# Performance work log

Measured on AMD Instinct MI355X. Metric: run time of the kernel, lower is better.

Reference implementation:

```python
import jax, jax.numpy as jnp
import numpy as np

N_NODES = 1_000_000
N_EDGES = 5_000_000
N_GRAPHS = 4096
HIDDEN = 16


def transform(x):
    # Transform wrapper: fn=tanh, then nan_to_num(nan=0, posinf=10, neginf=-10).clamp(-10, 10)
    y = jnp.tanh(x)
    y = jnp.nan_to_num(y, nan=0.0, posinf=10.0, neginf=-10.0)
    return jnp.clip(y, -10.0, 10.0)


def setup_inputs() -> dict:
    key = jax.random.key(0)
    ks = jax.random.split(key, 10)
    x = jax.random.normal(ks[0], (N_NODES, 3), dtype=jnp.float32)
    edge_index = jax.random.randint(ks[1], (2, N_EDGES), 0, N_NODES, dtype=jnp.int32)
    batch = jnp.sort(jax.random.randint(ks[2], (N_NODES,), 0, N_GRAPHS, dtype=jnp.int32))
    s1 = 1.0 / np.sqrt(3.0)
    s2 = 1.0 / np.sqrt(HIDDEN)
    s3 = 1.0 / np.sqrt(2 * HIDDEN)
    w1 = jax.random.uniform(ks[3], (3, HIDDEN), jnp.float32, -s1, s1)
    b1 = jax.random.uniform(ks[4], (HIDDEN,), jnp.float32, -s1, s1)
    w2 = jax.random.uniform(ks[5], (HIDDEN, HIDDEN), jnp.float32, -s2, s2)
    b2 = jax.random.uniform(ks[6], (HIDDEN,), jnp.float32, -s2, s2)
    w3 = jax.random.uniform(ks[7], (2 * HIDDEN, 1), jnp.float32, -s3, s3)
    b3 = jax.random.uniform(ks[8], (1,), jnp.float32, -s3, s3)
    return {"x": x, "edge_index": edge_index, "batch": batch,
            "w1": w1, "b1": b1, "w2": w2, "b2": b2, "w3": w3, "b3": b3}


def reference(x, edge_index, batch, w1, b1, w2, b2, w3, b3):
    n_nodes = x.shape[0]
    h = transform(x @ w1 + b1)                                  # [N, H]
    row, col = edge_index[0], edge_index[1]
    # degree of each destination node (row), clamped to >= 1
    deg = jax.ops.segment_sum(jnp.ones((row.shape[0],), x.dtype), row,
                              num_segments=n_nodes)             # [N]
    deg = jnp.maximum(deg, 1.0)
    # gather source features, scatter-add to destinations, normalize
    agg = jax.ops.segment_sum(h[col], row, num_segments=n_nodes)  # [N, H]
    agg = agg / deg[:, None]
    h = transform(agg @ w2 + b2)                                # [N, H]
    # per-graph mean and max pooling
    cnt = jax.ops.segment_sum(jnp.ones((n_nodes,), x.dtype), batch,
                              num_segments=N_GRAPHS)            # [G]
    h_sum = jax.ops.segment_sum(h, batch, num_segments=N_GRAPHS)  # [G, H]
    h_mean = h_sum / jnp.maximum(cnt, 1.0)[:, None]
    h_max = jax.ops.segment_max(h, batch, num_segments=N_GRAPHS)  # [G, H]
    h_max = jnp.where(jnp.isneginf(h_max), 0.0, h_max)
    pooled = jnp.concatenate([h_mean, h_max], axis=1)           # [G, 2H]
    out = jax.nn.sigmoid(pooled @ w3 + b3)                      # [G, 1]
    return out.squeeze(-1)
```

## Files before the change

kernel.cpp:

```cpp
#include <hip/hip_runtime.h>
#include <hip/hip_bf16.h>
#include <hip/hip_fp16.h>

static constexpr int NN = 1000000;
static constexpr int NE = 5000000;
static constexpr int NG = 4096;
static constexpr int BIN_SH = 8;
static constexpr int BIN_SZ = 1 << BIN_SH;
static constexpr int NB = (NN + BIN_SZ - 1) >> BIN_SH;
static constexpr int CAP_SH = 11;
static constexpr int CAP = 1 << CAP_SH;
static constexpr int EPB = 16384;
static constexpr int EPW = EPB / 1024;
static constexpr int BIN_BLOCKS = (NE + EPB - 1) / EPB;
static constexpr int CHUNK = 512;
static constexpr float KEXP = 2.8853900817779268f;

__device__ __forceinline__ float exp2_fast(float x) {
#if __has_builtin(__builtin_amdgcn_exp2f)
    return __builtin_amdgcn_exp2f(x);
#else
    return exp2f(x);
#endif
}

__device__ __forceinline__ float tanh_scaled(float s) {
    float e = exp2_fast(s);
    return fmaf(-2.0f, __frcp_rn(e + 1.0f), 1.0f);
}

__device__ __forceinline__ float fast_tanh(float x) {
    float e = __expf(2.0f * x);
    return 1.0f - 2.0f * __fdividef(1.0f, e + 1.0f);
}

__global__ __launch_bounds__(1024) void bin_scatter_k(
    const int* __restrict__ row, const int* __restrict__ col,
    const float* __restrict__ x,
    int* __restrict__ binCursor, unsigned int* __restrict__ pack,
    __half* __restrict__ xh)
{
    __shared__ int hist[NB];
    for (int i = blockIdx.x * 1024 + threadIdx.x; i < NN; i += BIN_BLOCKS * 1024) {
        union { __half2 h2[2]; uint2 u; } o;
        o.h2[0] = __floats2half2_rn(x[3 * i + 0], x[3 * i + 1]);
        o.h2[1] = __floats2half2_rn(x[3 * i + 2], 0.0f);
        *reinterpret_cast<uint2*>(xh + 4 * (size_t)i) = o.u;
    }

    for (int i = threadIdx.x; i < NB; i += 1024) hist[i] = 0;
    __syncthreads();
    int base = blockIdx.x * EPB;

    int r[EPW], c[EPW];
    bool val[EPW];
#pragma unroll
    for (int k = 0; k < EPW; ++k) {
        int e = base + k * 1024 + threadIdx.x;
        val[k] = e < NE;
        r[k] = val[k] ? row[e] : 0;
        c[k] = val[k] ? col[e] : 0;
    }
#pragma unroll
    for (int k = 0; k < EPW; ++k)
        if (val[k]) atomicAdd(&hist[r[k] >> BIN_SH], 1);
    __syncthreads();
    for (int i = threadIdx.x; i < NB; i += 1024) {
        int cc = hist[i];
        hist[i] = cc ? ((i << CAP_SH) + atomicAdd(&binCursor[i], cc)) : 0;
    }
    __syncthreads();
    int pos[EPW];
#pragma unroll
    for (int k = 0; k < EPW; ++k)
        if (val[k]) pos[k] = atomicAdd(&hist[r[k] >> BIN_SH], 1);
#pragma unroll
    for (int k = 0; k < EPW; ++k)
        if (val[k]) pack[pos[k]] = ((unsigned int)(r[k] & (BIN_SZ - 1)) << 20)
                                   | (unsigned int)c[k];
}

#define PREFETCH_CHUNK(CS2, GX0, GX1, RL0, RL1)                                   \
    {                                                                             \
        RL0 = RL1 = -1;                                                           \
        int cs2_ = (CS2);                                                         \
        if (cs2_ < ee) {                                                          \
            int mm_ = min(CHUNK, ee - cs2_);                                      \
            int o0_ = tid, o1_ = 256 + tid;                                       \
            if (o0_ < mm_) {                                                      \
                unsigned int p_ = pack[cs2_ + o0_];                               \
                RL0 = (int)(p_ >> 20);                                            \
                GX0 = *reinterpret_cast<const uint2*>(xh + 4 * (size_t)(p_ & 0xFFFFFu)); \
            }                                                                     \
            if (o1_ < mm_) {                                                      \
                unsigned int p_ = pack[cs2_ + o1_];                               \
                RL1 = (int)(p_ >> 20);                                            \
                GX1 = *reinterpret_cast<const uint2*>(xh + 4 * (size_t)(p_ & 0xFFFFFu)); \
            }                                                                     \
        }                                                                         \
    }

__global__ __launch_bounds__(256) void bucket_agg_k(
    const unsigned int* __restrict__ pack,
    const int* __restrict__ binCursor,
    const __half* __restrict__ xh,
    const int* __restrict__ batch,
    const float* __restrict__ w1,
    const float* __restrict__ b1,
    const float* __restrict__ w2,
    const float* __restrict__ b2,
    float* __restrict__ h_sum,
    unsigned int* __restrict__ h_max,
    int* __restrict__ cnt)
{
    __shared__ uint4 pay[CHUNK * 2];
    __shared__ int scnt[BIN_SZ];
    __shared__ int sstart[BIN_SZ];
    __shared__ int wsum[4];

    int tid = threadIdx.x;
    int lane = tid & 63, wid = tid >> 6;
    int b = blockIdx.x;
    int nodeBase = b << BIN_SH;
    int nNodes = min(BIN_SZ, NN - nodeBase);
    int es = b << CAP_SH;
    int ee = es + binCursor[b];

    float b1s[16];
#pragma unroll
    for (int j = 0; j < 16; ++j) b1s[j] = b1[j] * KEXP;

    __half2 acc8[8];
#pragma unroll
    for (int q = 0; q < 8; ++q) acc8[q] = __half2half2(__float2half(0.0f));
    int dg = 0;

    uint2 gxA0, gxA1, gxB0, gxB1;
    int rlA0, rlA1, rlB0, rlB1;
    PREFETCH_CHUNK(es,          gxA0, gxA1, rlA0, rlA1);
    PREFETCH_CHUNK(es + CHUNK,  gxB0, gxB1, rlB0, rlB1);

    for (int cs = es; cs < ee; cs += CHUNK) {
        int m = min(CHUNK, ee - cs);
        scnt[tid] = 0;
        __syncthreads();

        if (rlA0 >= 0) atomicAdd(&scnt[rlA0], 1);
        if (rlA1 >= 0) atomicAdd(&scnt[rlA1], 1);

        uint2 gxC0, gxC1;
        int rlC0, rlC1;
        PREFETCH_CHUNK(cs + 2 * CHUNK, gxC0, gxC1, rlC0, rlC1);
        __syncthreads();

        int v = scnt[tid];
        int sc = v;
#pragma unroll
        for (int off = 1; off < 64; off <<= 1) {
            int u = __shfl_up(sc, off);
            if (lane >= off) sc += u;
        }
        if (lane == 63) wsum[wid] = sc;
        __syncthreads();
        int pre = 0;
#pragma unroll
        for (int w = 0; w < 4; ++w) pre += (w < wid) ? wsum[w] : 0;
        int ex = pre + sc - v;
        sstart[tid] = ex;
        scnt[tid] = ex;
        __syncthreads();

#pragma unroll
        for (int k = 0; k < 2; ++k) {
            int rlk = k ? rlA1 : rlA0;
            if (rlk >= 0) {
                union { uint2 u; __half2 h2[2]; } xi;
                xi.u = k ? gxA1 : gxA0;
                float2 x01 = __half22float2(xi.h2[0]);
                float xs0 = x01.x * KEXP;
                float xs1 = x01.y * KEXP;
                float xs2 = __low2float(xi.h2[1]) * KEXP;
                union { __half2 h2[8]; uint4 u[2]; } o;
#pragma unroll
                for (int q = 0; q < 8; ++q) {
                    float va = fmaf(xs2, w1[32 + 2 * q], fmaf(xs1, w1[16 + 2 * q],
                               fmaf(xs0, w1[2 * q], b1s[2 * q])));
                    float vb = fmaf(xs2, w1[33 + 2 * q], fmaf(xs1, w1[17 + 2 * q],
                               fmaf(xs0, w1[2 * q + 1], b1s[2 * q + 1])));
                    o.h2[q] = __floats2half2_rn(tanh_scaled(va), tanh_scaled(vb));
                }
                int pos = atomicAdd(&scnt[rlk], 1);
                pay[2 * pos + 0] = o.u[0];
                pay[2 * pos + 1] = o.u[1];
            }
        }
        __syncthreads();

        if (tid < nNodes) {
            int s0 = sstart[tid];
            int e0 = (tid < 255) ? sstart[tid + 1] : m;
            dg += e0 - s0;
            for (int e = s0; e < e0; ++e) {
                union { uint4 u; __half2 h2[4]; } ua, ub;
                ua.u = pay[2 * e + 0];
                ub.u = pay[2 * e + 1];
#pragma unroll
                for (int q = 0; q < 4; ++q) {
                    acc8[q] = __hadd2(acc8[q], ua.h2[q]);
                    acc8[4 + q] = __hadd2(acc8[4 + q], ub.h2[q]);
                }
            }
        }
        __syncthreads();

        gxA0 = gxB0; gxA1 = gxB1; rlA0 = rlB0; rlA1 = rlB1;
        gxB0 = gxC0; gxB1 = gxC1; rlB0 = rlC0; rlB1 = rlC1;
    }

    if (tid < nNodes) {
        float acc[16];
#pragma unroll
        for (int q = 0; q < 8; ++q) {
            float2 f = __half22float2(acc8[q]);
            acc[2 * q + 0] = f.x;
            acc[2 * q + 1] = f.y;
        }
        float inv = 1.0f / fmaxf((float)dg, 1.0f);
        float s[16];
#pragma unroll
        for (int j = 0; j < 16; ++j) s[j] = b2[j];
#pragma unroll
        for (int k = 0; k < 16; ++k) {
            float a = acc[k] * inv;
#pragma unroll
            for (int j = 0; j < 16; ++j) s[j] = fmaf(a, w2[16 * k + j], s[j]);
        }
        float m[16];
#pragma unroll
        for (int j = 0; j < 16; ++j) { s[j] = fast_tanh(s[j]); m[j] = s[j]; }

        int g = batch[nodeBase + tid];
        int gp = __shfl_up(g, 1);
        int head = (lane == 0) || (g != gp);
        unsigned long long hm = __ballot(head != 0);

        int f = head;
#pragma unroll
        for (int off = 1; off < 64; off <<= 1) {
            int fu = __shfl_up(f, off);
            bool take = (lane >= off) && (f == 0);
#pragma unroll
            for (int j = 0; j < 16; ++j) {
                float su = __shfl_up(s[j], off);
                float mu = __shfl_up(m[j], off);
                if (take) { s[j] += su; m[j] = fmaxf(m[j], mu); }
            }
            if (lane >= off) f |= fu;
        }

        int hnext = __shfl_down(head, 1);
        bool is_last = (lane == 63) || (hnext != 0);
        if (is_last) {
            unsigned long long below = hm & (~0ULL >> (63 - lane));
            int start = 63 - __clzll(below);
            int seglen = lane - start + 1;
#pragma unroll
            for (int j = 0; j < 16; ++j) {
                unsafeAtomicAdd(&h_sum[16 * g + j], s[j]);
                atomicMax(&h_max[16 * g + j], __float_as_uint(m[j] + 2.0f));
            }
            atomicAdd(&cnt[g], seglen);
        }
    }
}

__global__ __launch_bounds__(256) void out_k(
    const float* __restrict__ h_sum,
    const unsigned int* __restrict__ h_max,
    const int* __restrict__ cnt,
    const float* __restrict__ w3,
    const float* __restrict__ b3,
    float* __restrict__ out)
{
    int g = blockIdx.x * 256 + threadIdx.x;
    if (g >= NG) return;
    float invc = 1.0f / fmaxf((float)cnt[g], 1.0f);
    float acc = b3[0];
#pragma unroll
    for (int j = 0; j < 16; ++j) {
        float mean = h_sum[16 * g + j] * invc;
        unsigned int e = h_max[16 * g + j];
        float mx = (e == 0u) ? 0.0f : (__uint_as_float(e) - 2.0f);
        acc = fmaf(mean, w3[j], fmaf(mx, w3[16 + j], acc));
    }
    out[g] = 1.0f / (1.0f + __expf(-acc));
}

extern "C" void kernel_launch(void* const* d_in, const int* in_sizes, int n_in,
                              void* d_out, int out_size, void* d_ws, size_t ws_size,
                              hipStream_t stream)
{
    const float* x   = (const float*)d_in[0];
    const int*   ei  = (const int*)d_in[1];
    const int*   bat = (const int*)d_in[2];
    const float* w1  = (const float*)d_in[3];
    const float* b1  = (const float*)d_in[4];
    const float* w2  = (const float*)d_in[5];
    const float* b2  = (const float*)d_in[6];
    const float* w3  = (const float*)d_in[7];
    const float* b3  = (const float*)d_in[8];
    float* out = (float*)d_out;

    char* ws = (char*)d_ws;
    size_t off = 0;
    int* binCursor = (int*)(ws + off);         off += 16384;
    float* h_sum  = (float*)(ws + off);        off += (size_t)NG * 16 * 4;
    unsigned int* h_max = (unsigned int*)(ws + off); off += (size_t)NG * 16 * 4;
    int* cnt      = (int*)(ws + off);          off += (size_t)NG * 4;
    size_t zero_bytes = off;
    unsigned int* pack = (unsigned int*)(ws + off); off += (size_t)NB * CAP * 4;
    __half* xh    = (__half*)(ws + off);       off += (size_t)NN * 4 * 2;

    hipMemsetAsync(d_ws, 0, zero_bytes, stream);

    bin_scatter_k<<<BIN_BLOCKS, 1024, 0, stream>>>(ei, ei + NE, x, binCursor, pack, xh);
    bucket_agg_k<<<NB, 256, 0, stream>>>(pack, binCursor, xh, bat,
                                         w1, b1, w2, b2, h_sum, h_max, cnt);
    out_k<<<(NG + 255) / 256, 256, 0, stream>>>(h_sum, h_max, cnt, w3, b3, out);
}
```

Baseline: 187.5 us.

## Process each node bin with a single wavefront instead of a whole block

Each 256-node bin is now handled by one 64-lane wavefront, with four bins per block. Each wave has private LDS scratch, and every block-wide __syncthreads is replaced by a wave barrier. Each lane handles four nodes, chunks shrink to 128 edges, and the prefix scan over bin counts becomes a single-wave scan over int4 groups. This removes block-level synchronisation, at the cost of more serial work per lane, more registers for four accumulators, and load imbalance between waves within a block.

```diff
diff --git a/kernel.cpp b/kernel.cpp
--- a/kernel.cpp
+++ b/kernel.cpp
@@ -13,7 +13,7 @@
 static constexpr int EPB = 16384;
 static constexpr int EPW = EPB / 1024;
 static constexpr int BIN_BLOCKS = (NE + EPB - 1) / EPB;
-static constexpr int CHUNK = 512;
+static constexpr int CHUNKW = 128;
 static constexpr float KEXP = 2.8853900817779268f;
 
 __device__ __forceinline__ float exp2_fast(float x) {
@@ -80,20 +80,19 @@
                                    | (unsigned int)c[k];
 }
 
-#define PREFETCH_CHUNK(CS2, GX0, GX1, RL0, RL1)                                   \
+#define PREFETCH_W(CS2, GX0, GX1, RL0, RL1)                                       \
     {                                                                             \
         RL0 = RL1 = -1;                                                           \
         int cs2_ = (CS2);                                                         \
         if (cs2_ < ee) {                                                          \
-            int mm_ = min(CHUNK, ee - cs2_);                                      \
-            int o0_ = tid, o1_ = 256 + tid;                                       \
-            if (o0_ < mm_) {                                                      \
-                unsigned int p_ = pack[cs2_ + o0_];                               \
+            int mm_ = min(CHUNKW, ee - cs2_);                                     \
+            if (lane < mm_) {                                                     \
+                unsigned int p_ = pack[cs2_ + lane];                              \
                 RL0 = (int)(p_ >> 20);                                            \
                 GX0 = *reinterpret_cast<const uint2*>(xh + 4 * (size_t)(p_ & 0xFFFFFu)); \
             }                                                                     \
-            if (o1_ < mm_) {                                                      \
-                unsigned int p_ = pack[cs2_ + o1_];                               \
+            if (64 + lane < mm_) {                                                \
+                unsigned int p_ = pack[cs2_ + 64 + lane];                         \
                 RL1 = (int)(p_ >> 20);                                            \
                 GX1 = *reinterpret_cast<const uint2*>(xh + 4 * (size_t)(p_ & 0xFFFFFu)); \
             }                                                                     \
@@ -113,14 +112,18 @@
     unsigned int* __restrict__ h_max,
     int* __restrict__ cnt)
 {
-    __shared__ uint4 pay[CHUNK * 2];
-    __shared__ int scnt[BIN_SZ];
-    __shared__ int sstart[BIN_SZ];
-    __shared__ int wsum[4];
+    __shared__ uint4 payA[4][CHUNKW * 2];
+    __shared__ int scntA[4][BIN_SZ];
+    __shared__ int sstartA[4][BIN_SZ];
 
     int tid = threadIdx.x;
     int lane = tid & 63, wid = tid >> 6;
-    int b = blockIdx.x;
+    uint4* pay = payA[wid];
+    int* scnt = scntA[wid];
+    int* sstart = sstartA[wid];
+
+    int b = blockIdx.x * 4 + wid;
+    if (b >= NB) return;
     int nodeBase = b << BIN_SH;
     int nNodes = min(BIN_SZ, NN - nodeBase);
     int es = b << CAP_SH;
@@ -130,45 +133,47 @@
 #pragma unroll
     for (int j = 0; j < 16; ++j) b1s[j] = b1[j] * KEXP;
 
-    __half2 acc8[8];
-#pragma unroll
-    for (int q = 0; q < 8; ++q) acc8[q] = __half2half2(__float2half(0.0f));
-    int dg = 0;
+    __half2 acc[4][8];
+#pragma unroll
+    for (int k = 0; k < 4; ++k)
+#pragma unroll
+        for (int q = 0; q < 8; ++q) acc[k][q] = __half2half2(__float2half(0.0f));
+    int dg[4] = {0, 0, 0, 0};
 
     uint2 gxA0, gxA1, gxB0, gxB1;
     int rlA0, rlA1, rlB0, rlB1;
-    PREFETCH_CHUNK(es,          gxA0, gxA1, rlA0, rlA1);
-    PREFETCH_CHUNK(es + CHUNK,  gxB0, gxB1, rlB0, rlB1);
-
-    for (int cs = es; cs < ee; cs += CHUNK) {
-        int m = min(CHUNK, ee - cs);
-        scnt[tid] = 0;
-        __syncthreads();
-
+    PREFETCH_W(es,           gxA0, gxA1, rlA0, rlA1);
+    PREFETCH_W(es + CHUNKW,  gxB0, gxB1, rlB0, rlB1);
+
+    for (int cs = es; cs < ee; cs += CHUNKW) {
+        int m = min(CHUNKW, ee - cs);
+
+        *reinterpret_cast<int4*>(&scnt[4 * lane]) = make_int4(0, 0, 0, 0);
         if (rlA0 >= 0) atomicAdd(&scnt[rlA0], 1);
         if (rlA1 >= 0) atomicAdd(&scnt[rlA1], 1);
 
         uint2 gxC0, gxC1;
         int rlC0, rlC1;
-        PREFETCH_CHUNK(cs + 2 * CHUNK, gxC0, gxC1, rlC0, rlC1);
-        __syncthreads();
-
-        int v = scnt[tid];
-        int sc = v;
+        PREFETCH_W(cs + 2 * CHUNKW, gxC0, gxC1, rlC0, rlC1);
+
+        __builtin_amdgcn_wave_barrier();
+        int4 v4 = *reinterpret_cast<int4*>(&scnt[4 * lane]);
+        int tsum = v4.x + v4.y + v4.z + v4.w;
+        int sc = tsum;
 #pragma unroll
         for (int off = 1; off < 64; off <<= 1) {
             int u = __shfl_up(sc, off);
             if (lane >= off) sc += u;
         }
-        if (lane == 63) wsum[wid] = sc;
-        __syncthreads();
-        int pre = 0;
-#pragma unroll
-        for (int w = 0; w < 4; ++w) pre += (w < wid) ? wsum[w] : 0;
-        int ex = pre + sc - v;
-        sstart[tid] = ex;
-        scnt[tid] = ex;
-        __syncthreads();
+        int ex = sc - tsum;
+        int4 st;
+        st.x = ex;
+        st.y = st.x + v4.x;
+        st.z = st.y + v4.y;
+        st.w = st.z + v4.z;
+        *reinterpret_cast<int4*>(&sstart[4 * lane]) = st;
+        *reinterpret_cast<int4*>(&scnt[4 * lane]) = st;
+        __builtin_amdgcn_wave_barrier();
 
 #pragma unroll
         for (int k = 0; k < 2; ++k) {
@@ -194,52 +199,58 @@
                 pay[2 * pos + 1] = o.u[1];
             }
         }
-        __syncthreads();
-
-        if (tid < nNodes) {
-            int s0 = sstart[tid];
-            int e0 = (tid < 255) ? sstart[tid + 1] : m;
-            dg += e0 - s0;
-            for (int e = s0; e < e0; ++e) {
-                union { uint4 u; __half2 h2[4]; } ua, ub;
-                ua.u = pay[2 * e + 0];
-                ub.u = pay[2 * e + 1];
-#pragma unroll
-                for (int q = 0; q < 4; ++q) {
-                    acc8[q] = __hadd2(acc8[q], ua.h2[q]);
-                    acc8[4 + q] = __hadd2(acc8[4 + q], ub.h2[q]);
+        __builtin_amdgcn_wave_barrier();
+
+#pragma unroll
+        for (int k = 0; k < 4; ++k) {
+            int node = 64 * k + lane;
+            if (node < nNodes) {
+                int s0 = sstart[node];
+                int e0 = (node < 255) ? sstart[node + 1] : m;
+                dg[k] += e0 - s0;
+                for (int e = s0; e < e0; ++e) {
+                    union { uint4 u; __half2 h2[4]; } ua, ub;
+                    ua.u = pay[2 * e + 0];
+                    ub.u = pay[2 * e + 1];
+#pragma unroll
+                    for (int q = 0; q < 4; ++q) {
+                        acc[k][q] = __hadd2(acc[k][q], ua.h2[q]);
+                        acc[k][4 + q] = __hadd2(acc[k][4 + q], ub.h2[q]);
+                    }
                 }
             }
         }
-        __syncthreads();
+        __builtin_amdgcn_wave_barrier();
 
         gxA0 = gxB0; gxA1 = gxB1; rlA0 = rlB0; rlA1 = rlB1;
         gxB0 = gxC0; gxB1 = gxC1; rlB0 = rlC0; rlB1 = rlC1;
     }
 
-    if (tid < nNodes) {
-        float acc[16];
+#pragma unroll
+    for (int k = 0; k < 4; ++k) {
+        if (64 * k >= nNodes) break;
+        float af[16];
 #pragma unroll
         for (int q = 0; q < 8; ++q) {
-            float2 f = __half22float2(acc8[q]);
-            acc[2 * q + 0] = f.x;
-            acc[2 * q + 1] = f.y;
-        }
-        float inv = 1.0f / fmaxf((float)dg, 1.0f);
+            float2 f = __half22float2(acc[k][q]);
+            af[2 * q + 0] = f.x;
+            af[2 * q + 1] = f.y;
+        }
+        float inv = 1.0f / fmaxf((float)dg[k], 1.0f);
         float s[16];
 #pragma unroll
         for (int j = 0; j < 16; ++j) s[j] = b2[j];
 #pragma unroll
-        for (int k = 0; k < 16; ++k) {
-            float a = acc[k] * inv;
-#pragma unroll
-            for (int j = 0; j < 16; ++j) s[j] = fmaf(a, w2[16 * k + j], s[j]);
-        }
-        float m[16];
-#pragma unroll
-        for (int j = 0; j < 16; ++j) { s[j] = fast_tanh(s[j]); m[j] = s[j]; }
-
-        int g = batch[nodeBase + tid];
+        for (int kk = 0; kk < 16; ++kk) {
+            float a = af[kk] * inv;
+#pragma unroll
+            for (int j = 0; j < 16; ++j) s[j] = fmaf(a, w2[16 * kk + j], s[j]);
+        }
+        float mx[16];
+#pragma unroll
+        for (int j = 0; j < 16; ++j) { s[j] = fast_tanh(s[j]); mx[j] = s[j]; }
+
+        int g = batch[nodeBase + 64 * k + lane];
         int gp = __shfl_up(g, 1);
         int head = (lane == 0) || (g != gp);
         unsigned long long hm = __ballot(head != 0);
@@ -252,8 +263,8 @@
 #pragma unroll
             for (int j = 0; j < 16; ++j) {
                 float su = __shfl_up(s[j], off);
-                float mu = __shfl_up(m[j], off);
-                if (take) { s[j] += su; m[j] = fmaxf(m[j], mu); }
+                float mu = __shfl_up(mx[j], off);
+                if (take) { s[j] += su; mx[j] = fmaxf(mx[j], mu); }
             }
             if (lane >= off) f |= fu;
         }
@@ -267,7 +278,7 @@
 #pragma unroll
             for (int j = 0; j < 16; ++j) {
                 unsafeAtomicAdd(&h_sum[16 * g + j], s[j]);
-                atomicMax(&h_max[16 * g + j], __float_as_uint(m[j] + 2.0f));
+                atomicMax(&h_max[16 * g + j], __float_as_uint(mx[j] + 2.0f));
             }
             atomicAdd(&cnt[g], seglen);
         }
@@ -324,7 +335,7 @@
     hipMemsetAsync(d_ws, 0, zero_bytes, stream);
 
     bin_scatter_k<<<BIN_BLOCKS, 1024, 0, stream>>>(ei, ei + NE, x, binCursor, pack, xh);
-    bucket_agg_k<<<NB, 256, 0, stream>>>(pack, binCursor, xh, bat,
-                                         w1, b1, w2, b2, h_sum, h_max, cnt);
+    bucket_agg_k<<<(NB + 3) / 4, 256, 0, stream>>>(pack, binCursor, xh, bat,
+                                                   w1, b1, w2, b2, h_sum, h_max, cnt);
     out_k<<<(NG + 255) / 256, 256, 0, stream>>>(h_sum, h_max, cnt, w3, b3, out);
 }
```

Measured after the change: 290.6 us. 55.0% more time.
